# Kernel optimization log

Hardware: AMD Instinct MI355X
Metric: run time of the kernel (lower is better)

The kernel has to match this reference:

```python
import jax, jax.numpy as jnp
import numpy as np

NUM_SEGMENTS = 65536  # number of unique voxels (max index in unq_inv + 1)


def setup_inputs() -> dict:
    key = jax.random.key(0)
    k1, k2 = jax.random.split(key)
    feat = jax.random.normal(k1, (1000000, 128), dtype=jnp.float32)
    unq_inv = jax.random.randint(k2, (1000000,), 0, NUM_SEGMENTS, dtype=jnp.int64 if jax.config.jax_enable_x64 else jnp.int32)
    return {"feat": feat, "unq_inv": unq_inv, "mode": 1}


def reference(feat, unq_inv, mode):
    # mode: 1 -> max, 2 -> mean, 3 -> sum (matches scatter_all.symbolic encoding)
    if mode == 1:
        out = jax.ops.segment_max(feat, unq_inv, num_segments=NUM_SEGMENTS)
        # torch_scatter leaves empty segments at 0; jax fills with -inf -> fix up
        counts = jax.ops.segment_sum(jnp.ones((feat.shape[0],), feat.dtype), unq_inv, num_segments=NUM_SEGMENTS)
        out = jnp.where(counts[:, None] > 0, out, jnp.zeros((), feat.dtype))
    elif mode == 2:
        s = jax.ops.segment_sum(feat, unq_inv, num_segments=NUM_SEGMENTS)
        counts = jax.ops.segment_sum(jnp.ones((feat.shape[0],), feat.dtype), unq_inv, num_segments=NUM_SEGMENTS)
        out = s / jnp.maximum(counts, 1.0)[:, None]
    else:
        out = jax.ops.segment_sum(feat, unq_inv, num_segments=NUM_SEGMENTS)
    return out
```

## Files before the change

### kernel.cpp

```cpp
#include <hip/hip_runtime.h>
#include <math.h>

#define NEG_INF_BITS 0xFF800000u
#define SCAN_B 1024

typedef float f32x4_t __attribute__((ext_vector_type(4)));

__device__ __forceinline__ float4 ld_nt4(const float4* p) {
    f32x4_t v = __builtin_nontemporal_load((const f32x4_t*)p);
    return make_float4(v[0], v[1], v[2], v[3]);
}
__device__ __forceinline__ void st_nt4(float4* p, float4 v) {
    f32x4_t x = {v.x, v.y, v.z, v.w};
    __builtin_nontemporal_store(x, (f32x4_t*)p);
}


__global__ void zero_counts_kernel(int* __restrict__ counts, int nseg) {
    const int i = blockIdx.x * blockDim.x + threadIdx.x;
    if (i < nseg) counts[i] = 0;
}

__global__ void hist_rank_kernel(const int* __restrict__ inv,
                                 int* __restrict__ counts,
                                 int* __restrict__ rank, int n) {
    const int stride = gridDim.x * blockDim.x;
    const int n4 = n >> 2;
    const int4* inv4 = (const int4*)inv;
    int4* rank4 = (int4*)rank;
    for (int i = blockIdx.x * blockDim.x + threadIdx.x; i < n4; i += stride) {
        int4 s = inv4[i];
        int4 rk;
        rk.x = atomicAdd(&counts[s.x], 1);
        rk.y = atomicAdd(&counts[s.y], 1);
        rk.z = atomicAdd(&counts[s.z], 1);
        rk.w = atomicAdd(&counts[s.w], 1);
        rank4[i] = rk;
    }
    if (blockIdx.x == 0 && threadIdx.x < (n & 3)) {
        int i = (n4 << 2) + threadIdx.x;
        rank[i] = atomicAdd(&counts[inv[i]], 1);
    }
}

__global__ __launch_bounds__(SCAN_B)
void scan_reduce_kernel(const int* __restrict__ counts,
                        int* __restrict__ bsum, int nseg) {
    __shared__ int lds[SCAN_B / 64];
    const int t = threadIdx.x;
    const int idx = blockIdx.x * SCAN_B + t;
    int v = (idx < nseg) ? counts[idx] : 0;
    for (int off = 32; off > 0; off >>= 1) v += __shfl_down(v, off, 64);
    if ((t & 63) == 0) lds[t >> 6] = v;
    __syncthreads();
    if (t < SCAN_B / 64) {
        int s = lds[t];
        for (int off = SCAN_B / 128; off > 0; off >>= 1) s += __shfl_down(s, off, 64);
        if (t == 0) bsum[blockIdx.x] = s;
    }
}

__global__ __launch_bounds__(SCAN_B)
void scan_top_kernel(int* __restrict__ bsum, int* __restrict__ offsets,
                     int nblk, int nseg) {
    __shared__ int lds[SCAN_B];
    const int t = threadIdx.x;
    int v = (t < nblk) ? bsum[t] : 0;
    lds[t] = v;
    __syncthreads();
    for (int off = 1; off < SCAN_B; off <<= 1) {
        int x = lds[t];
        int add = (t >= off) ? lds[t - off] : 0;
        __syncthreads();
        lds[t] = x + add;
        __syncthreads();
    }
    if (t < nblk) bsum[t] = lds[t] - v;
    if (t == nblk - 1) offsets[nseg] = lds[t];
}

__global__ __launch_bounds__(SCAN_B)
void scan_down_kernel(const int* __restrict__ counts,
                      const int* __restrict__ bsum,
                      int* __restrict__ offsets, int nseg) {
    __shared__ int lds[SCAN_B];
    const int t = threadIdx.x;
    const int idx = blockIdx.x * SCAN_B + t;
    int c = (idx < nseg) ? counts[idx] : 0;
    lds[t] = c;
    __syncthreads();
    for (int off = 1; off < SCAN_B; off <<= 1) {
        int x = lds[t];
        int add = (t >= off) ? lds[t - off] : 0;
        __syncthreads();
        lds[t] = x + add;
        __syncthreads();
    }
    if (idx < nseg) offsets[idx] = bsum[blockIdx.x] + lds[t] - c;
}

__global__ void scatteridx_kernel(const int* __restrict__ inv,
                                  const int* __restrict__ rank,
                                  const int* __restrict__ offsets,
                                  int* __restrict__ rowidx, int n) {
    const int stride = gridDim.x * blockDim.x;
    const int n4 = n >> 2;
    const int4* inv4 = (const int4*)inv;
    const int4* rank4 = (const int4*)rank;
    for (int i = blockIdx.x * blockDim.x + threadIdx.x; i < n4; i += stride) {
        int4 s  = inv4[i];
        int4 rk = rank4[i];
        int base = i << 2;
        rowidx[offsets[s.x] + rk.x] = base + 0;
        rowidx[offsets[s.y] + rk.y] = base + 1;
        rowidx[offsets[s.z] + rk.z] = base + 2;
        rowidx[offsets[s.w] + rk.w] = base + 3;
    }
    if (blockIdx.x == 0 && threadIdx.x < (n & 3)) {
        int i = (n4 << 2) + threadIdx.x;
        rowidx[offsets[inv[i]] + rank[i]] = i;
    }
}

__global__ void seg_reduce_kernel(const float4* __restrict__ feat4,
                                  const int* __restrict__ rowidx,
                                  const int* __restrict__ offsets,
                                  float4* __restrict__ out4,
                                  int nseg,
                                  const int* __restrict__ mode_p) {
    const int mode = mode_p[0];
    const int t = blockIdx.x * blockDim.x + threadIdx.x;
    const int g = t >> 5;
    const int q = t & 31;
    if (g >= nseg) return;

    const int start = offsets[g];
    const int end   = offsets[g + 1];

    float4 acc;
    if (mode == 1) {
        acc = make_float4(-INFINITY, -INFINITY, -INFINITY, -INFINITY);
        int r = start;
        for (; r + 8 <= end; r += 8) {
            int rows[8];
            #pragma unroll
            for (int k = 0; k < 8; ++k) rows[k] = rowidx[r + k];
            float4 v[8];
            #pragma unroll
            for (int k = 0; k < 8; ++k) v[k] = ld_nt4(feat4 + (size_t)rows[k] * 32 + q);
            #pragma unroll
            for (int k = 0; k < 8; ++k) {
                acc.x = fmaxf(acc.x, v[k].x);
                acc.y = fmaxf(acc.y, v[k].y);
                acc.z = fmaxf(acc.z, v[k].z);
                acc.w = fmaxf(acc.w, v[k].w);
            }
        }
        for (; r + 4 <= end; r += 4) {
            int rows[4];
            #pragma unroll
            for (int k = 0; k < 4; ++k) rows[k] = rowidx[r + k];
            float4 v[4];
            #pragma unroll
            for (int k = 0; k < 4; ++k) v[k] = ld_nt4(feat4 + (size_t)rows[k] * 32 + q);
            #pragma unroll
            for (int k = 0; k < 4; ++k) {
                acc.x = fmaxf(acc.x, v[k].x);
                acc.y = fmaxf(acc.y, v[k].y);
                acc.z = fmaxf(acc.z, v[k].z);
                acc.w = fmaxf(acc.w, v[k].w);
            }
        }
        for (; r < end; r++) {
            const float4 v = ld_nt4(feat4 + (size_t)rowidx[r] * 32 + q);
            acc.x = fmaxf(acc.x, v.x); acc.y = fmaxf(acc.y, v.y);
            acc.z = fmaxf(acc.z, v.z); acc.w = fmaxf(acc.w, v.w);
        }
        if (end == start) acc = make_float4(0.f, 0.f, 0.f, 0.f);
    } else {
        acc = make_float4(0.f, 0.f, 0.f, 0.f);
        int r = start;
        for (; r + 8 <= end; r += 8) {
            int rows[8];
            #pragma unroll
            for (int k = 0; k < 8; ++k) rows[k] = rowidx[r + k];
            float4 v[8];
            #pragma unroll
            for (int k = 0; k < 8; ++k) v[k] = ld_nt4(feat4 + (size_t)rows[k] * 32 + q);
            #pragma unroll
            for (int k = 0; k < 8; ++k) {
                acc.x += v[k].x; acc.y += v[k].y; acc.z += v[k].z; acc.w += v[k].w;
            }
        }
        for (; r + 4 <= end; r += 4) {
            int rows[4];
            #pragma unroll
            for (int k = 0; k < 4; ++k) rows[k] = rowidx[r + k];
            float4 v[4];
            #pragma unroll
            for (int k = 0; k < 4; ++k) v[k] = ld_nt4(feat4 + (size_t)rows[k] * 32 + q);
            #pragma unroll
            for (int k = 0; k < 4; ++k) {
                acc.x += v[k].x; acc.y += v[k].y; acc.z += v[k].z; acc.w += v[k].w;
            }
        }
        for (; r < end; r++) {
            const float4 v = ld_nt4(feat4 + (size_t)rowidx[r] * 32 + q);
            acc.x += v.x; acc.y += v.y; acc.z += v.z; acc.w += v.w;
        }
        if (mode == 2) {
            const float c = fmaxf((float)(end - start), 1.0f);
            acc.x /= c; acc.y /= c; acc.z /= c; acc.w /= c;
        }
    }
    st_nt4(out4 + (size_t)g * 32 + q, acc);
}

__device__ __forceinline__ void atomicMaxFloat(float* addr, float val) {
    if (val >= 0.0f) atomicMax((int*)addr, __float_as_int(val));
    else             atomicMin((unsigned int*)addr, (unsigned int)__float_as_uint(val));
}

__global__ void fb_init_kernel(unsigned int* __restrict__ out, int out_n,
                               float* __restrict__ counts, int nseg,
                               const int* __restrict__ mode_p) {
    const int mode = mode_p[0];
    const unsigned int initv = (mode == 1) ? NEG_INF_BITS : 0u;
    const int stride = gridDim.x * blockDim.x;
    int i = blockIdx.x * blockDim.x + threadIdx.x;
    uint4* out4 = (uint4*)out;
    const int n4 = out_n >> 2;
    uint4 v4 = make_uint4(initv, initv, initv, initv);
    for (int j = i; j < n4; j += stride) out4[j] = v4;
    for (int j = i; j < nseg; j += stride) counts[j] = 0.0f;
}

__global__ void fb_scatter_kernel(const float4* __restrict__ feat4,
                                  const int* __restrict__ inv,
                                  float* __restrict__ out,
                                  float* __restrict__ counts,
                                  int nrows, const int* __restrict__ mode_p) {
    const int mode = mode_p[0];
    const int t = blockIdx.x * blockDim.x + threadIdx.x;
    const int row = t >> 5;
    const int q   = t & 31;
    if (row >= nrows) return;
    const int seg = inv[row];
    const float4 v = ((const float4*)feat4)[(size_t)row * 32 + q];
    float* dst = out + (size_t)seg * 128 + q * 4;
    if (mode == 1) {
        atomicMaxFloat(dst + 0, v.x); atomicMaxFloat(dst + 1, v.y);
        atomicMaxFloat(dst + 2, v.z); atomicMaxFloat(dst + 3, v.w);
        if (q == 0) atomicAdd(&counts[seg], 1.0f);
    } else {
        atomicAdd(dst + 0, v.x); atomicAdd(dst + 1, v.y);
        atomicAdd(dst + 2, v.z); atomicAdd(dst + 3, v.w);
        if (mode == 2 && q == 0) atomicAdd(&counts[seg], 1.0f);
    }
}

__global__ void fb_fixup_kernel(float* __restrict__ out, int out_n,
                                const float* __restrict__ counts,
                                const int* __restrict__ mode_p) {
    const int mode = mode_p[0];
    if (mode == 3) return;
    const int i = blockIdx.x * blockDim.x + threadIdx.x;
    if (i >= out_n) return;
    const int seg = i >> 7;
    const float c = counts[seg];
    if (mode == 1) { if (c == 0.0f) out[i] = 0.0f; }
    else           { out[i] = out[i] / fmaxf(c, 1.0f); }
}

extern "C" void kernel_launch(void* const* d_in, const int* in_sizes, int n_in,
                              void* d_out, int out_size, void* d_ws, size_t ws_size,
                              hipStream_t stream) {
    const float* feat   = (const float*)d_in[0];
    const int*   inv    = (const int*)d_in[1];
    const int*   mode_p = (const int*)d_in[2];
    float* out = (float*)d_out;

    const int nrows = in_sizes[1];
    const int nseg  = out_size / 128;
    const int nblk  = (nseg + SCAN_B - 1) / SCAN_B;

    const size_t need = (size_t)(nseg + (nseg + 1) + nrows + nblk + nrows) * sizeof(int);

    if (ws_size >= need && nblk <= SCAN_B) {
        int* counts  = (int*)d_ws;
        int* offsets = counts + nseg;
        int* rowidx  = offsets + (nseg + 1);
        int* bsum    = rowidx + nrows;
        int* rank    = bsum + nblk;

        {
            dim3 block(256), grid((nseg + 255) / 256);
            zero_counts_kernel<<<grid, block, 0, stream>>>(counts, nseg);
        }
        {
            dim3 block(256), grid(1024);
            hist_rank_kernel<<<grid, block, 0, stream>>>(inv, counts, rank, nrows);
        }
        scan_reduce_kernel<<<nblk, SCAN_B, 0, stream>>>(counts, bsum, nseg);
        scan_top_kernel<<<1, SCAN_B, 0, stream>>>(bsum, offsets, nblk, nseg);
        scan_down_kernel<<<nblk, SCAN_B, 0, stream>>>(counts, bsum, offsets, nseg);
        {
            dim3 block(256), grid(1024);
            scatteridx_kernel<<<grid, block, 0, stream>>>(inv, rank, offsets, rowidx, nrows);
        }
        {
            const long long total = (long long)nseg * 32;
            dim3 block(256), grid((unsigned int)((total + 255) / 256));
            seg_reduce_kernel<<<grid, block, 0, stream>>>((const float4*)feat, rowidx,
                                                          offsets, (float4*)out,
                                                          nseg, mode_p);
        }
    } else {
        float* counts = (float*)d_ws;
        {
            dim3 block(256), grid(2048);
            fb_init_kernel<<<grid, block, 0, stream>>>((unsigned int*)out, out_size,
                                                       counts, nseg, mode_p);
        }
        {
            const long long total = (long long)nrows * 32;
            dim3 block(256), grid((unsigned int)((total + 255) / 256));
            fb_scatter_kernel<<<grid, block, 0, stream>>>((const float4*)feat, inv,
                                                          out, counts, nrows, mode_p);
        }
        {
            dim3 block(256), grid((out_size + 255) / 256);
            fb_fixup_kernel<<<grid, block, 0, stream>>>(out, out_size, counts, mode_p);
        }
    }
}
```

Baseline: 172.7 us.

## Use full wavefront per segment with float2 lanes and shuffle-broadcast row indices

The segment reduce kernel now gives each segment a full 64-lane wavefront, each lane handling a float2 of the 128-wide row, instead of 32 lanes with float4. Row indices are loaded cooperatively, one per lane for up to 64 rows, then broadcast with __shfl, so redundant per-lane index loads go away. Loads are issued 16 rows at a time with predication to increase memory-level parallelism. This doubles the thread count and uses narrower 8-byte loads, which may lower per-instruction bandwidth efficiency.

```diff
diff --git a/kernel.cpp b/kernel.cpp
--- a/kernel.cpp
+++ b/kernel.cpp
@@ -4,15 +4,16 @@
 #define NEG_INF_BITS 0xFF800000u
 #define SCAN_B 1024
 
+typedef float f32x2_t __attribute__((ext_vector_type(2)));
 typedef float f32x4_t __attribute__((ext_vector_type(4)));
 
-__device__ __forceinline__ float4 ld_nt4(const float4* p) {
-    f32x4_t v = __builtin_nontemporal_load((const f32x4_t*)p);
-    return make_float4(v[0], v[1], v[2], v[3]);
-}
-__device__ __forceinline__ void st_nt4(float4* p, float4 v) {
-    f32x4_t x = {v.x, v.y, v.z, v.w};
-    __builtin_nontemporal_store(x, (f32x4_t*)p);
+__device__ __forceinline__ float2 ld_nt2(const float2* p) {
+    f32x2_t v = __builtin_nontemporal_load((const f32x2_t*)p);
+    return make_float2(v[0], v[1]);
+}
+__device__ __forceinline__ void st_nt2(float2* p, float2 v) {
+    f32x2_t x = {v.x, v.y};
+    __builtin_nontemporal_store(x, (f32x2_t*)p);
 }
 
 
@@ -122,98 +123,66 @@
     }
 }
 
-__global__ void seg_reduce_kernel(const float4* __restrict__ feat4,
-                                  const int* __restrict__ rowidx,
-                                  const int* __restrict__ offsets,
-                                  float4* __restrict__ out4,
-                                  int nseg,
-                                  const int* __restrict__ mode_p) {
+__global__ __launch_bounds__(256)
+void seg_reduce_kernel(const float2* __restrict__ feat2,
+                       const int* __restrict__ rowidx,
+                       const int* __restrict__ offsets,
+                       float2* __restrict__ out2,
+                       int nseg,
+                       const int* __restrict__ mode_p) {
     const int mode = mode_p[0];
     const int t = blockIdx.x * blockDim.x + threadIdx.x;
-    const int g = t >> 5;
-    const int q = t & 31;
+    const int g = t >> 6;
+    const int lane = t & 63;
     if (g >= nseg) return;
 
     const int start = offsets[g];
     const int end   = offsets[g + 1];
-
-    float4 acc;
-    if (mode == 1) {
-        acc = make_float4(-INFINITY, -INFINITY, -INFINITY, -INFINITY);
-        int r = start;
-        for (; r + 8 <= end; r += 8) {
-            int rows[8];
+    const int count = end - start;
+
+    const bool is_max = (mode == 1);
+    float2 acc = is_max ? make_float2(-INFINITY, -INFINITY) : make_float2(0.f, 0.f);
+
+    for (int base = start; base < end; base += 64) {
+        const int cnt = min(64, end - base);
+        const int myrow = (lane < cnt) ? rowidx[base + lane] : 0;
+
+        for (int kk = 0; kk < cnt; kk += 16) {
+            float2 v[16];
             #pragma unroll
-            for (int k = 0; k < 8; ++k) rows[k] = rowidx[r + k];
-            float4 v[8];
-            #pragma unroll
-            for (int k = 0; k < 8; ++k) v[k] = ld_nt4(feat4 + (size_t)rows[k] * 32 + q);
-            #pragma unroll
-            for (int k = 0; k < 8; ++k) {
-                acc.x = fmaxf(acc.x, v[k].x);
-                acc.y = fmaxf(acc.y, v[k].y);
-                acc.z = fmaxf(acc.z, v[k].z);
-                acc.w = fmaxf(acc.w, v[k].w);
+            for (int j = 0; j < 16; ++j) {
+                if (kk + j < cnt) {
+                    const int row = __shfl(myrow, kk + j, 64);
+                    v[j] = ld_nt2(feat2 + (size_t)row * 64 + lane);
+                }
             }
-        }
-        for (; r + 4 <= end; r += 4) {
-            int rows[4];
-            #pragma unroll
-            for (int k = 0; k < 4; ++k) rows[k] = rowidx[r + k];
-            float4 v[4];
-            #pragma unroll
-            for (int k = 0; k < 4; ++k) v[k] = ld_nt4(feat4 + (size_t)rows[k] * 32 + q);
-            #pragma unroll
-            for (int k = 0; k < 4; ++k) {
-                acc.x = fmaxf(acc.x, v[k].x);
-                acc.y = fmaxf(acc.y, v[k].y);
-                acc.z = fmaxf(acc.z, v[k].z);
-                acc.w = fmaxf(acc.w, v[k].w);
+            if (is_max) {
+                #pragma unroll
+                for (int j = 0; j < 16; ++j) {
+                    if (kk + j < cnt) {
+                        acc.x = fmaxf(acc.x, v[j].x);
+                        acc.y = fmaxf(acc.y, v[j].y);
+                    }
+                }
+            } else {
+                #pragma unroll
+                for (int j = 0; j < 16; ++j) {
+                    if (kk + j < cnt) {
+                        acc.x += v[j].x;
+                        acc.y += v[j].y;
+                    }
+                }
             }
         }
-        for (; r < end; r++) {
-            const float4 v = ld_nt4(feat4 + (size_t)rowidx[r] * 32 + q);
-            acc.x = fmaxf(acc.x, v.x); acc.y = fmaxf(acc.y, v.y);
-            acc.z = fmaxf(acc.z, v.z); acc.w = fmaxf(acc.w, v.w);
-        }
-        if (end == start) acc = make_float4(0.f, 0.f, 0.f, 0.f);
-    } else {
-        acc = make_float4(0.f, 0.f, 0.f, 0.f);
-        int r = start;
-        for (; r + 8 <= end; r += 8) {
-            int rows[8];
-            #pragma unroll
-            for (int k = 0; k < 8; ++k) rows[k] = rowidx[r + k];
-            float4 v[8];
-            #pragma unroll
-            for (int k = 0; k < 8; ++k) v[k] = ld_nt4(feat4 + (size_t)rows[k] * 32 + q);
-            #pragma unroll
-            for (int k = 0; k < 8; ++k) {
-                acc.x += v[k].x; acc.y += v[k].y; acc.z += v[k].z; acc.w += v[k].w;
-            }
-        }
-        for (; r + 4 <= end; r += 4) {
-            int rows[4];
-            #pragma unroll
-            for (int k = 0; k < 4; ++k) rows[k] = rowidx[r + k];
-            float4 v[4];
-            #pragma unroll
-            for (int k = 0; k < 4; ++k) v[k] = ld_nt4(feat4 + (size_t)rows[k] * 32 + q);
-            #pragma unroll
-            for (int k = 0; k < 4; ++k) {
-                acc.x += v[k].x; acc.y += v[k].y; acc.z += v[k].z; acc.w += v[k].w;
-            }
-        }
-        for (; r < end; r++) {
-            const float4 v = ld_nt4(feat4 + (size_t)rowidx[r] * 32 + q);
-            acc.x += v.x; acc.y += v.y; acc.z += v.z; acc.w += v.w;
-        }
-        if (mode == 2) {
-            const float c = fmaxf((float)(end - start), 1.0f);
-            acc.x /= c; acc.y /= c; acc.z /= c; acc.w /= c;
-        }
-    }
-    st_nt4(out4 + (size_t)g * 32 + q, acc);
+    }
+
+    if (count == 0) {
+        acc = make_float2(0.f, 0.f);
+    } else if (mode == 2) {
+        const float c = (float)count;
+        acc.x /= c; acc.y /= c;
+    }
+    st_nt2(out2 + (size_t)g * 64 + lane, acc);
 }
 
 __device__ __forceinline__ void atomicMaxFloat(float* addr, float val) {
@@ -246,7 +215,7 @@
     const int q   = t & 31;
     if (row >= nrows) return;
     const int seg = inv[row];
-    const float4 v = ((const float4*)feat4)[(size_t)row * 32 + q];
+    const float4 v = feat4[(size_t)row * 32 + q];
     float* dst = out + (size_t)seg * 128 + q * 4;
     if (mode == 1) {
         atomicMaxFloat(dst + 0, v.x); atomicMaxFloat(dst + 1, v.y);
@@ -309,10 +278,10 @@
             scatteridx_kernel<<<grid, block, 0, stream>>>(inv, rank, offsets, rowidx, nrows);
         }
         {
-            const long long total = (long long)nseg * 32;
+            const long long total = (long long)nseg * 64;
             dim3 block(256), grid((unsigned int)((total + 255) / 256));
-            seg_reduce_kernel<<<grid, block, 0, stream>>>((const float4*)feat, rowidx,
-                                                          offsets, (float4*)out,
+            seg_reduce_kernel<<<grid, block, 0, stream>>>((const float2*)feat, rowidx,
+                                                          offsets, (float2*)out,
                                                           nseg, mode_p);
         }
     } else {
```

New measurement: 203.3 us. 1.18x slower.
